# Optimization experiments

Measured on AMD Instinct MI355X. Metric: run time of the kernel, lower is better.

Reference implementation:

```python
import jax, jax.numpy as jnp
import numpy as np
import math

EPS = 1e-8


def _cdist(x, y):
    # torch.cdist(p=2) with a grad-safe sqrt (0 grad at zero distance)
    d2 = (jnp.sum(x * x, -1)[:, None] + jnp.sum(y * y, -1)[None, :]
          - 2.0 * x @ y.T)
    d2 = jnp.maximum(d2, 0.0)
    pos = d2 > 0
    return jnp.where(pos, jnp.sqrt(jnp.where(pos, d2, 1.0)), 0.0)


def _metric(proj, dim):
    # [B,D,D] rank-1 + identity, symmetrized, Frobenius-normalized
    m = jnp.einsum('bi,bj->bij', proj, proj) / dim
    m = m + jnp.eye(dim, dtype=proj.dtype)[None]
    m = 0.5 * (m + jnp.swapaxes(m, -2, -1))
    fro = jnp.sqrt(jnp.sum(m * m, axis=(-2, -1), keepdims=True))
    return m / (fro + EPS)


def setup_inputs() -> dict:
    key = jax.random.key(0)
    ks = jax.random.split(key, 4)
    B, D = 4096, 128
    return {
        'query_points': jax.random.normal(ks[0], (B, D), jnp.float32),
        'key_points': jax.random.normal(ks[1], (B, D), jnp.float32),
        'Wq': 0.1 * jax.random.normal(ks[2], (D, D), jnp.float32),
        'bq': jnp.zeros((D,), jnp.float32),
        'Wk': 0.1 * jax.random.normal(ks[3], (D, D), jnp.float32),
        'bk': jnp.zeros((D,), jnp.float32),
    }


def reference(query_points, key_points, Wq, bq, Wk, bk):
    D = Wq.shape[0]
    q = query_points @ Wq.T + bq  # [B,D]
    k = key_points @ Wk.T + bk    # [B,D]
    qm = _metric(q, D)            # [B,D,D]
    km = _metric(k, D)
    q_norm = jnp.sqrt(jnp.einsum('bi,bij,bj->b', q, qm, q))
    k_norm = jnp.sqrt(jnp.einsum('bi,bij,bj->b', k, km, k))
    qn = q / (q_norm[:, None] + EPS)
    kn = k / (k_norm[:, None] + EPS)
    dists = _cdist(qn, kn)                       # [B,B]
    sims = 1.0 / (1.0 + dists)
    temperature = math.sqrt(float(D))
    scores = jax.nn.softmax(sims * temperature, axis=-1)
    score_dists = _cdist(scores, scores)
    input_dists = _cdist(query_points, key_points)
    scale = jnp.mean(input_dists) / (jnp.mean(score_dists) + EPS)
    scores = scores * scale
    scores = scores / (jnp.sum(scores, axis=-1, keepdims=True) + EPS)
    return scores
```

## Files before the change

kernel.cpp:

```cpp
#include <hip/hip_runtime.h>
#include <hip/hip_bf16.h>
#include <math.h>

typedef short short8 __attribute__((ext_vector_type(8)));
typedef float floatx4 __attribute__((ext_vector_type(4)));

#define NB 4096
#define DD 128
static constexpr float EPSF = 1e-8f;
static constexpr float TEMP = 11.313708498984760390f;

static __device__ __forceinline__ short f2bf(float f) {
    __hip_bfloat16 h = __float2bfloat16(f);
    union { __hip_bfloat16 h; short s; } u; u.h = h; return u.s;
}
static __device__ __forceinline__ float bf2f(short s) {
    union { __hip_bfloat16 h; short s; } u; u.s = s;
    return __bfloat162float(u.h);
}

static __device__ __forceinline__ short8 load_cvt8(const float* __restrict__ p) {
    float4 a = *(const float4*)p;
    float4 b = *(const float4*)(p + 4);
    short8 o;
    o[0] = f2bf(a.x); o[1] = f2bf(a.y); o[2] = f2bf(a.z); o[3] = f2bf(a.w);
    o[4] = f2bf(b.x); o[5] = f2bf(b.y); o[6] = f2bf(b.z); o[7] = f2bf(b.w);
    return o;
}

static __device__ __forceinline__ int frag_off(int g, int kidx) {
    return ((((g >> 4) * 4 + (kidx >> 5)) * 4 + ((kidx >> 3) & 3)) * 16
            + (g & 15)) * 8 + (kidx & 7);
}

__global__ __launch_bounds__(512) void proj_kernel(
    const float* __restrict__ qp, const float* __restrict__ kp,
    const float* __restrict__ Wq, const float* __restrict__ bq,
    const float* __restrict__ Wk, const float* __restrict__ bk,
    __hip_bfloat16* __restrict__ qn, __hip_bfloat16* __restrict__ kn,
    float* __restrict__ rq, float* __restrict__ rk)
{
    int t = threadIdx.x;
    int b = blockIdx.x;

    int which = b >> 8;
    int row0 = (b & 255) * 16;
    const float* x    = which ? kp : qp;
    const float* W    = which ? Wk : Wq;
    const float* bias = which ? bk : bq;
    short* outv = which ? (short*)kn : (short*)qn;
    float* outr = which ? rk : rq;

    int lane = t & 63, wid = t >> 6;
    int m = lane & 15, quad = lane >> 4;
    int colb = wid * 16;

    floatx4 acc = (floatx4){0.f, 0.f, 0.f, 0.f};

    #pragma unroll
    for (int ks = 0; ks < 4; ++ks) {
        int koff = ks * 32 + quad * 8;
        short8 af  = load_cvt8(x + (row0 + m) * DD + koff);
        short8 bfr = load_cvt8(W + (colb + m) * DD + koff);
        acc = __builtin_amdgcn_mfma_f32_16x16x32_bf16(af, bfr, acc, 0, 0, 0);
    }

    __shared__ float buf[8][16];
    __shared__ float nfb[16];

    float bv = bias[colb + m];

    #pragma unroll
    for (int r = 0; r < 4; ++r) {
        float v = acc[r] + bv;
        acc[r] = v;
        float p = v * v;
        p += __shfl_xor(p, 1); p += __shfl_xor(p, 2);
        p += __shfl_xor(p, 4); p += __shfl_xor(p, 8);
        if (m == 0) buf[wid][quad*4 + r] = p;
    }
    __syncthreads();
    if (t < 16) {
        float s = 0.f;
        #pragma unroll
        for (int w = 0; w < 8; ++w) s += buf[w][t];
        float fro = sqrtf(s*s*(1.0f/16384.0f) + s*(1.0f/64.0f) + 128.0f);
        float qnorm = sqrtf((s*s*(1.0f/128.0f) + s) / (fro + EPSF));
        nfb[t] = 1.0f / (qnorm + EPSF);
    }
    __syncthreads();

    #pragma unroll
    for (int r = 0; r < 4; ++r) {
        int lrow = quad*4 + r;
        int g = row0 + lrow;
        float nf = nfb[lrow];
        float v = acc[r] * nf;
        short sb = f2bf(v);
        outv[frag_off(g, colb + m)] = sb;
        float vf = bf2f(sb);
        float u = vf * vf;
        u += __shfl_xor(u, 1); u += __shfl_xor(u, 2);
        u += __shfl_xor(u, 4); u += __shfl_xor(u, 8);
        if (m == 0) buf[wid][lrow] = u;
    }
    __syncthreads();
    if (t < 16) {
        float s = 0.f;
        #pragma unroll
        for (int w = 0; w < 8; ++w) s += buf[w][t];
        outr[row0 + t] = s;
    }
}

__global__ __launch_bounds__(1024, 4) void score_rows(
    const __hip_bfloat16* __restrict__ qn, const __hip_bfloat16* __restrict__ kn,
    const float* __restrict__ rq, const float* __restrict__ rk,
    float* __restrict__ P)
{
    int lane = threadIdx.x & 63;
    int wid  = threadIdx.x >> 6;
    int m    = lane & 15;
    int quad = lane >> 4;

    int rowblk = blockIdx.x;
    int r0 = rowblk * 16;
    int cs = wid * 256;

    const short* qs  = (const short*)qn;
    const short* kks = (const short*)kn;

    short8 af[4];
    #pragma unroll
    for (int k4 = 0; k4 < 4; ++k4)
        af[k4] = *(const short8*)(qs + ((rowblk*4 + k4)*64 + lane)*8);

    float rqv = rq[r0 + m];

    floatx4 acc[4][4];
    float rs = 0.f;

    #pragma unroll
    for (int it = 0; it < 4; ++it) {
        #pragma unroll
        for (int ct = 0; ct < 4; ++ct) {
            int colblk = (cs >> 4) + it*4 + ct;
            short8 bfr[4];
            #pragma unroll
            for (int k4 = 0; k4 < 4; ++k4)
                bfr[k4] = *(const short8*)(kks + ((colblk*4 + k4)*64 + lane)*8);
            floatx4 a = (floatx4){0.f, 0.f, 0.f, 0.f};
            #pragma unroll
            for (int k4 = 0; k4 < 4; ++k4)
                a = __builtin_amdgcn_mfma_f32_16x16x32_bf16(bfr[k4], af[k4], a, 0, 0, 0);
            floatx4 rkv = *(const floatx4*)(rk + colblk*16 + quad*4);
            #pragma unroll
            for (int r = 0; r < 4; ++r) {
                float d2 = fmaf(-2.0f, a[r], rqv + rkv[r]);
                float d  = d2 > 0.0f ? __builtin_amdgcn_sqrtf(d2) : 0.0f;
                float e  = __expf(TEMP * __builtin_amdgcn_rcpf(1.0f + d));
                a[r] = e;
                rs += e;
            }
            acc[it][ct] = a;
        }
    }

    rs += __shfl_xor(rs, 16);
    rs += __shfl_xor(rs, 32);

    __shared__ float sums[16][16];
    __shared__ float inv[16];
    if (lane < 16) sums[wid][lane] = rs;
    __syncthreads();
    if (threadIdx.x < 16) {
        float s = 0.f;
        #pragma unroll
        for (int w = 0; w < 16; ++w) s += sums[w][threadIdx.x];
        inv[threadIdx.x] = __builtin_amdgcn_rcpf(s + EPSF);
    }
    __syncthreads();

    float invv = inv[m];

    #pragma unroll
    for (int it = 0; it < 4; ++it) {
        #pragma unroll
        for (int ct = 0; ct < 4; ++ct) {
            floatx4 o = acc[it][ct] * invv;
            *(floatx4*)(P + (size_t)(r0 + m) * NB
                          + cs + it*64 + ct*16 + quad*4) = o;
        }
    }
}

extern "C" void kernel_launch(void* const* d_in, const int* in_sizes, int n_in,
                              void* d_out, int out_size, void* d_ws, size_t ws_size,
                              hipStream_t stream) {
    const float* qp = (const float*)d_in[0];
    const float* kp = (const float*)d_in[1];
    const float* Wq = (const float*)d_in[2];
    const float* bq = (const float*)d_in[3];
    const float* Wk = (const float*)d_in[4];
    const float* bk = (const float*)d_in[5];
    float* P = (float*)d_out;

    char* ws = (char*)d_ws;
    __hip_bfloat16* qn = (__hip_bfloat16*)ws;
    __hip_bfloat16* kn = (__hip_bfloat16*)(ws + (size_t)NB*DD*2);
    float* rq = (float*)(ws + (size_t)NB*DD*4);
    float* rk = (float*)(ws + (size_t)NB*DD*4 + (size_t)NB*4);

    hipLaunchKernelGGL(proj_kernel, dim3(512), dim3(512), 0, stream,
                       qp, kp, Wq, bq, Wk, bk, qn, kn, rq, rk);
    hipLaunchKernelGGL(score_rows, dim3(256), dim3(1024), 0, stream,
                       qn, kn, rq, rk, P);
}
```

Measured before the change: 119.3 us.

## Fuse projection and score kernels with a grid-wide atomic barrier

Merges the projection/normalization kernel and the row-score softmax kernel into one persistent launch of 256 blocks. Each block first does two projection units, then all blocks wait at a global atomic counter barrier before computing scores. This removes one kernel launch and the gap between kernels, but adds a memset launch and spin-waiting. It relies on all 256 blocks being resident at the same time to avoid deadlock.

```diff
diff --git a/kernel.cpp b/kernel.cpp
--- a/kernel.cpp
+++ b/kernel.cpp
@@ -7,6 +7,7 @@
 
 #define NB 4096
 #define DD 128
+#define NBLK 256
 static constexpr float EPSF = 1e-8f;
 static constexpr float TEMP = 11.313708498984760390f;
 
@@ -33,95 +34,103 @@
             + (g & 15)) * 8 + (kidx & 7);
 }
 
-__global__ __launch_bounds__(512) void proj_kernel(
+__global__ __launch_bounds__(1024, 4) void fused_kernel(
     const float* __restrict__ qp, const float* __restrict__ kp,
     const float* __restrict__ Wq, const float* __restrict__ bq,
     const float* __restrict__ Wk, const float* __restrict__ bk,
     __hip_bfloat16* __restrict__ qn, __hip_bfloat16* __restrict__ kn,
-    float* __restrict__ rq, float* __restrict__ rk)
+    float* __restrict__ rq, float* __restrict__ rk,
+    float* __restrict__ P, unsigned* __restrict__ ctr)
 {
-    int t = threadIdx.x;
-    int b = blockIdx.x;
-
-    int which = b >> 8;
-    int row0 = (b & 255) * 16;
-    const float* x    = which ? kp : qp;
-    const float* W    = which ? Wk : Wq;
-    const float* bias = which ? bk : bq;
-    short* outv = which ? (short*)kn : (short*)qn;
-    float* outr = which ? rk : rq;
-
-    int lane = t & 63, wid = t >> 6;
-    int m = lane & 15, quad = lane >> 4;
-    int colb = wid * 16;
-
-    floatx4 acc = (floatx4){0.f, 0.f, 0.f, 0.f};
-
-    #pragma unroll
-    for (int ks = 0; ks < 4; ++ks) {
-        int koff = ks * 32 + quad * 8;
-        short8 af  = load_cvt8(x + (row0 + m) * DD + koff);
-        short8 bfr = load_cvt8(W + (colb + m) * DD + koff);
-        acc = __builtin_amdgcn_mfma_f32_16x16x32_bf16(af, bfr, acc, 0, 0, 0);
-    }
-
-    __shared__ float buf[8][16];
-    __shared__ float nfb[16];
-
-    float bv = bias[colb + m];
-
-    #pragma unroll
-    for (int r = 0; r < 4; ++r) {
-        float v = acc[r] + bv;
-        acc[r] = v;
-        float p = v * v;
-        p += __shfl_xor(p, 1); p += __shfl_xor(p, 2);
-        p += __shfl_xor(p, 4); p += __shfl_xor(p, 8);
-        if (m == 0) buf[wid][quad*4 + r] = p;
-    }
-    __syncthreads();
-    if (t < 16) {
-        float s = 0.f;
-        #pragma unroll
-        for (int w = 0; w < 8; ++w) s += buf[w][t];
-        float fro = sqrtf(s*s*(1.0f/16384.0f) + s*(1.0f/64.0f) + 128.0f);
-        float qnorm = sqrtf((s*s*(1.0f/128.0f) + s) / (fro + EPSF));
-        nfb[t] = 1.0f / (qnorm + EPSF);
-    }
-    __syncthreads();
-
-    #pragma unroll
-    for (int r = 0; r < 4; ++r) {
-        int lrow = quad*4 + r;
-        int g = row0 + lrow;
-        float nf = nfb[lrow];
-        float v = acc[r] * nf;
-        short sb = f2bf(v);
-        outv[frag_off(g, colb + m)] = sb;
-        float vf = bf2f(sb);
-        float u = vf * vf;
-        u += __shfl_xor(u, 1); u += __shfl_xor(u, 2);
-        u += __shfl_xor(u, 4); u += __shfl_xor(u, 8);
-        if (m == 0) buf[wid][lrow] = u;
-    }
-    __syncthreads();
-    if (t < 16) {
-        float s = 0.f;
-        #pragma unroll
-        for (int w = 0; w < 8; ++w) s += buf[w][t];
-        outr[row0 + t] = s;
-    }
-}
-
-__global__ __launch_bounds__(1024, 4) void score_rows(
-    const __hip_bfloat16* __restrict__ qn, const __hip_bfloat16* __restrict__ kn,
-    const float* __restrict__ rq, const float* __restrict__ rk,
-    float* __restrict__ P)
-{
-    int lane = threadIdx.x & 63;
-    int wid  = threadIdx.x >> 6;
+    int tid  = threadIdx.x;
+    int lane = tid & 63;
+    int wid  = tid >> 6;
     int m    = lane & 15;
     int quad = lane >> 4;
+
+    __shared__ float buf[2][8][16];
+    __shared__ float nfb[2][16];
+
+    {
+        int g    = wid >> 3;
+        int wid8 = wid & 7;
+        int u    = blockIdx.x * 2 + g;
+
+        int which = u >> 8;
+        int row0 = (u & 255) * 16;
+        const float* x    = which ? kp : qp;
+        const float* W    = which ? Wk : Wq;
+        const float* bias = which ? bk : bq;
+        short* outv = which ? (short*)kn : (short*)qn;
+        float* outr = which ? rk : rq;
+
+        int colb = wid8 * 16;
+
+        floatx4 acc = (floatx4){0.f, 0.f, 0.f, 0.f};
+
+        #pragma unroll
+        for (int ks = 0; ks < 4; ++ks) {
+            int koff = ks * 32 + quad * 8;
+            short8 af  = load_cvt8(x + (row0 + m) * DD + koff);
+            short8 bfr = load_cvt8(W + (colb + m) * DD + koff);
+            acc = __builtin_amdgcn_mfma_f32_16x16x32_bf16(af, bfr, acc, 0, 0, 0);
+        }
+
+        float bv = bias[colb + m];
+
+        #pragma unroll
+        for (int r = 0; r < 4; ++r) {
+            float v = acc[r] + bv;
+            acc[r] = v;
+            float p = v * v;
+            p += __shfl_xor(p, 1); p += __shfl_xor(p, 2);
+            p += __shfl_xor(p, 4); p += __shfl_xor(p, 8);
+            if (m == 0) buf[g][wid8][quad*4 + r] = p;
+        }
+        __syncthreads();
+        if (wid8 == 0 && lane < 16) {
+            float s = 0.f;
+            #pragma unroll
+            for (int w = 0; w < 8; ++w) s += buf[g][w][lane];
+            float fro = sqrtf(s*s*(1.0f/16384.0f) + s*(1.0f/64.0f) + 128.0f);
+            float qnorm = sqrtf((s*s*(1.0f/128.0f) + s) / (fro + EPSF));
+            nfb[g][lane] = 1.0f / (qnorm + EPSF);
+        }
+        __syncthreads();
+
+        #pragma unroll
+        for (int r = 0; r < 4; ++r) {
+            int lrow = quad*4 + r;
+            int gg = row0 + lrow;
+            float nf = nfb[g][lrow];
+            float v = acc[r] * nf;
+            short sb = f2bf(v);
+            outv[frag_off(gg, colb + m)] = sb;
+            float vf = bf2f(sb);
+            float u2 = vf * vf;
+            u2 += __shfl_xor(u2, 1); u2 += __shfl_xor(u2, 2);
+            u2 += __shfl_xor(u2, 4); u2 += __shfl_xor(u2, 8);
+            if (m == 0) buf[g][wid8][lrow] = u2;
+        }
+        __syncthreads();
+        if (wid8 == 0 && lane < 16) {
+            float s = 0.f;
+            #pragma unroll
+            for (int w = 0; w < 8; ++w) s += buf[g][w][lane];
+            outr[row0 + lane] = s;
+        }
+    }
+
+    __syncthreads();
+    if (tid == 0) {
+        __hip_atomic_fetch_add(ctr, 1u, __ATOMIC_RELEASE,
+                               __HIP_MEMORY_SCOPE_AGENT);
+        while (__hip_atomic_load(ctr, __ATOMIC_ACQUIRE,
+                                 __HIP_MEMORY_SCOPE_AGENT) < (unsigned)NBLK) {
+            __builtin_amdgcn_s_sleep(2);
+        }
+    }
+    __syncthreads();
 
     int rowblk = blockIdx.x;
     int r0 = rowblk * 16;
@@ -173,11 +182,11 @@
     __shared__ float inv[16];
     if (lane < 16) sums[wid][lane] = rs;
     __syncthreads();
-    if (threadIdx.x < 16) {
+    if (tid < 16) {
         float s = 0.f;
         #pragma unroll
-        for (int w = 0; w < 16; ++w) s += sums[w][threadIdx.x];
-        inv[threadIdx.x] = __builtin_amdgcn_rcpf(s + EPSF);
+        for (int w = 0; w < 16; ++w) s += sums[w][tid];
+        inv[tid] = __builtin_amdgcn_rcpf(s + EPSF);
     }
     __syncthreads();
 
@@ -210,9 +219,10 @@
     __hip_bfloat16* kn = (__hip_bfloat16*)(ws + (size_t)NB*DD*2);
     float* rq = (float*)(ws + (size_t)NB*DD*4);
     float* rk = (float*)(ws + (size_t)NB*DD*4 + (size_t)NB*4);
-
-    hipLaunchKernelGGL(proj_kernel, dim3(512), dim3(512), 0, stream,
-                       qp, kp, Wq, bq, Wk, bk, qn, kn, rq, rk);
-    hipLaunchKernelGGL(score_rows, dim3(256), dim3(1024), 0, stream,
-                       qn, kn, rq, rk, P);
-}
+    unsigned* ctr = (unsigned*)(ws + (size_t)NB*DD*4 + (size_t)NB*8);
+
+    hipMemsetAsync(ctr, 0, sizeof(unsigned), stream);
+
+    hipLaunchKernelGGL(fused_kernel, dim3(NBLK), dim3(1024), 0, stream,
+                       qp, kp, Wq, bq, Wk, bk, qn, kn, rq, rk, P, ctr);
+}
```

Measured after the change: 131.3 us. 10.0% more time.
